# Performance work log

Measured on AMD Instinct MI355X. Metric: run time of the kernel, lower is better.

Reference implementation:

```python
import jax, jax.numpy as jnp
import numpy as np

LN_EPS = 1e-5

def layernorm(x, w, b):
    mu = jnp.mean(x, axis=-1, keepdims=True)
    var = jnp.mean(jnp.square(x - mu), axis=-1, keepdims=True)
    return (x - mu) * jax.lax.rsqrt(var + LN_EPS) * w + b

def l2_normalize(x, eps=1e-12):
    n = jnp.sqrt(jnp.sum(jnp.square(x), axis=-1, keepdims=True))
    return x / jnp.maximum(n, eps)

def setup_inputs() -> dict:
    key = jax.random.key(0)
    k1, k2 = jax.random.split(key)
    B, D, Npix = 8, 64, 32768
    K, P = 19, 5
    return {
        "base_feature": jax.random.normal(k1, (B, D, Npix), dtype=jnp.float32),
        "means": jax.random.normal(k2, (K, P, D), dtype=jnp.float32) * 0.02,  # trunc_normal_(std=0.02)
        "diagonal": jnp.ones((K, P, D), dtype=jnp.float32),
        "feat_w": jnp.ones((D,), dtype=jnp.float32),
        "feat_b": jnp.zeros((D,), dtype=jnp.float32),
        "mask_w": jnp.ones((K,), dtype=jnp.float32),
        "mask_b": jnp.zeros((K,), dtype=jnp.float32),
    }

def gmm_log_prob(x, mu, scale):
    # x: [N, D]; mu, scale: [KP, D]  (MultivariateNormalDiag with scale_diag=scale)
    # log p = -0.5 * sum(((x-mu)/s)^2) - sum(log s) - 0.5*D*log(2*pi)
    D = x.shape[-1]
    inv2 = 1.0 / jnp.square(scale)                      # [KP, D]
    quad = (jnp.square(x) @ inv2.T                       # [N, KP]
            - 2.0 * (x @ (mu * inv2).T)
            + jnp.sum(jnp.square(mu) * inv2, axis=-1))
    log_norm = jnp.sum(jnp.log(scale), axis=-1) + 0.5 * D * jnp.log(2.0 * jnp.pi)
    return -0.5 * quad - log_norm                        # [N, KP]

def reference(base_feature, means, diagonal, feat_w, feat_b, mask_w, mask_b):
    B, D, Npix = base_feature.shape
    K, P, _ = means.shape
    # 'b c n -> (b n) c'
    _c = jnp.transpose(base_feature, (0, 2, 1)).reshape(B * Npix, D)
    _c = layernorm(_c, feat_w, feat_b)
    _c = l2_normalize(_c)
    means_n = l2_normalize(means)                        # means.data.copy_(l2_normalize(means))
    logp = gmm_log_prob(_c, means_n.reshape(K * P, D), diagonal.reshape(K * P, D))
    final_probs = logp.reshape(-1, K, P)                 # [(b n), K, P]
    _m_prob = jnp.max(final_probs, axis=-1)              # amax over components -> [(b n), K]
    out_seg = layernorm(_m_prob, mask_w, mask_b)         # mask_norm
    # '(b n) k -> b k n'
    out_seg = jnp.transpose(out_seg.reshape(B, Npix, K), (0, 2, 1))
    return out_seg
```

## Files before the change

### kernel.cpp

```cpp
#include <hip/hip_runtime.h>
#include <math.h>

#define BB    8
#define DD    64
#define NPIX  32768
#define KK    19
#define PP    5
#define KP    95
#define KPAD  96

typedef _Float16 half8 __attribute__((ext_vector_type(8)));
typedef float f32x4 __attribute__((ext_vector_type(4)));

#define ROW_B   528
#define SLOT_B  8448
#define UT_B    33792
#define SCR_OFF 33792
#define LDS_B   36352

__global__ __launch_bounds__(64) void gmm_prep(
        const float* __restrict__ means, const float* __restrict__ diag,
        const float* __restrict__ feat_w, const float* __restrict__ feat_b,
        _Float16* __restrict__ Ch, _Float16* __restrict__ Cl,
        float* __restrict__ cst, float* __restrict__ scal) {
    int j = blockIdx.x;
    int d = threadIdx.x;
    if (j < KP) {
        float mu = means[j * DD + d];
        float sc = diag[j * DD + d];
        float ss = mu * mu;
        #pragma unroll
        for (int off = 32; off; off >>= 1) ss += __shfl_xor(ss, off);
        float inv = 1.f / fmaxf(sqrtf(ss), 1e-12f);
        float mn = mu * inv;
        float i2 = 1.f / (sc * sc);
        float A = mn * i2;
        float B = -0.5f * i2;
        _Float16 ah = (_Float16)A; _Float16 al = (_Float16)(A - (float)ah);
        _Float16 bh = (_Float16)B; _Float16 bl = (_Float16)(B - (float)bh);
        Ch[j * 128 + 2 * d]     = ah;
        Ch[j * 128 + 2 * d + 1] = bh;
        Cl[j * 128 + 2 * d]     = al;
        Cl[j * 128 + 2 * d + 1] = bl;
        float c1 = mn * mn * i2;
        float c2 = logf(sc);
        #pragma unroll
        for (int off = 32; off; off >>= 1) {
            c1 += __shfl_xor(c1, off);
            c2 += __shfl_xor(c2, off);
        }
        if (d == 0) cst[j] = -0.5f * c1 - c2 - 58.8120661251f;
    } else {
        Ch[95 * 128 + 2 * d] = (_Float16)0.f; Ch[95 * 128 + 2 * d + 1] = (_Float16)0.f;
        Cl[95 * 128 + 2 * d] = (_Float16)0.f; Cl[95 * 128 + 2 * d + 1] = (_Float16)0.f;
        float w = feat_w[d], b = feat_b[d];
        float s0 = w * w, s1 = w * b, s2 = b * b;
        #pragma unroll
        for (int off = 32; off; off >>= 1) {
            s0 += __shfl_xor(s0, off);
            s1 += __shfl_xor(s1, off);
            s2 += __shfl_xor(s2, off);
        }
        if (d == 0) { cst[95] = 0.f; scal[0] = s0; scal[1] = s1; scal[2] = s2; }
    }
}

__global__ __launch_bounds__(128, 2) void gmm_main(
        const float* __restrict__ bf,
        const float* __restrict__ feat_w, const float* __restrict__ feat_b,
        const float* __restrict__ mask_w, const float* __restrict__ mask_b,
        const _Float16* __restrict__ Ch, const _Float16* __restrict__ Cl,
        const float* __restrict__ cst, const float* __restrict__ scal,
        float* __restrict__ out) {
    __shared__ __align__(16) unsigned char smem[LDS_B];
    float* scratch = (float*)(smem + SCR_OFF);

    const int tid  = threadIdx.x;
    const int w    = tid >> 6;
    const int lane = tid & 63;
    const int m15  = lane & 15;
    const int q    = lane >> 4;
    const int bidx = blockIdx.x;
    const int b    = bidx >> 9;
    const int n0   = (bidx & 511) << 6;

    half8 Ahf[3][4], Alf[3][4];
    #pragma unroll
    for (int t = 0; t < 3; ++t) {
        const int row = (3 * w + t) * 16 + m15;
        #pragma unroll
        for (int ks = 0; ks < 4; ++ks) {
            Ahf[t][ks] = *(const half8*)(Ch + row * 128 + ks * 32 + q * 8);
            Alf[t][ks] = *(const half8*)(Cl + row * 128 + ks * 32 + q * 8);
        }
    }

    const int dbase = w * 32;
    const float* xp = bf + (size_t)b * (DD * NPIX) + (size_t)dbase * NPIX + n0 + lane;
    float xs[32];
    #pragma unroll
    for (int i = 0; i < 32; ++i) xs[i] = xp[(size_t)i * NPIX];

    float S1 = 0.f, S2 = 0.f, S3 = 0.f, S4 = 0.f, S5 = 0.f;
    #pragma unroll
    for (int i = 0; i < 32; ++i) {
        float wd = feat_w[dbase + i];
        float bd = feat_b[dbase + i];
        float x  = xs[i];
        float t  = wd * x;
        S1 += x;
        S2 = fmaf(x, x, S2);
        S3 = fmaf(t, t, S3);
        S4 = fmaf(t, wd, S4);
        S5 = fmaf(t, bd, S5);
    }
    scratch[w * 320 +   0 + lane] = S1;
    scratch[w * 320 +  64 + lane] = S2;
    scratch[w * 320 + 128 + lane] = S3;
    scratch[w * 320 + 192 + lane] = S4;
    scratch[w * 320 + 256 + lane] = S5;
    __syncthreads();
    {
        const int ow = (1 - w) * 320;
        S1 += scratch[ow +   0 + lane];
        S2 += scratch[ow +  64 + lane];
        S3 += scratch[ow + 128 + lane];
        S4 += scratch[ow + 192 + lane];
        S5 += scratch[ow + 256 + lane];
    }
    const float W2 = scal[0], WB = scal[1], B2 = scal[2];
    float mu  = S1 * (1.f / 64.f);
    float var = fmaxf(S2 * (1.f / 64.f) - mu * mu, 0.f);
    float r   = rsqrtf(var + 1e-5f);
    float Sy2 = r * r * (S3 - 2.f * mu * S4 + mu * mu * W2)
              + 2.f * r * (S5 - mu * WB) + B2;
    float nrm  = sqrtf(fmaxf(Sy2, 0.f));
    float invn = 1.f / fmaxf(nrm, 1e-12f);
    float alpha = invn * r;
    float e = invn;
    float f = -alpha * mu;

    {
        unsigned char* rowp = smem + lane * ROW_B;
        #pragma unroll
        for (int g = 0; g < 8; ++g) {
            half8 vh, vl;
            #pragma unroll
            for (int jj = 0; jj < 4; ++jj) {
                int d = dbase + 4 * g + jj;
                float wd = feat_w[d];
                float bd = feat_b[d];
                float c  = fmaf(f, wd, e * bd);
                float u  = fmaf(alpha * wd, xs[4 * g + jj], c);
                float us = u * u;
                _Float16 uh = (_Float16)u;  _Float16 ul = (_Float16)(u  - (float)uh);
                _Float16 qh = (_Float16)us; _Float16 ql = (_Float16)(us - (float)qh);
                vh[2 * jj] = uh; vh[2 * jj + 1] = qh;
                vl[2 * jj] = ul; vl[2 * jj + 1] = ql;
            }
            *(half8*)(rowp + 4 * (dbase + 4 * g))       = vh;
            *(half8*)(rowp + 256 + 4 * (dbase + 4 * g)) = vl;
        }
    }
    __syncthreads();

    #pragma unroll 1
    for (int s = 0; s < 4; ++s) {
        const unsigned ubase = (unsigned)(s * 16 + m15) * ROW_B + q * 16;
        half8 Uh[4], Ul[4];
        #pragma unroll
        for (int ks = 0; ks < 4; ++ks) {
            Uh[ks] = *(const half8*)(smem + ubase + ks * 64);
            Ul[ks] = *(const half8*)(smem + ubase + 256 + ks * 64);
        }
        __syncthreads();

        f32x4 a0 = {0.f, 0.f, 0.f, 0.f}, a1 = a0, a2 = a0;
        #pragma unroll
        for (int ks = 0; ks < 4; ++ks) {
            a0 = __builtin_amdgcn_mfma_f32_16x16x32_f16(Ahf[0][ks], Uh[ks], a0, 0, 0, 0);
            a1 = __builtin_amdgcn_mfma_f32_16x16x32_f16(Ahf[1][ks], Uh[ks], a1, 0, 0, 0);
            a2 = __builtin_amdgcn_mfma_f32_16x16x32_f16(Ahf[2][ks], Uh[ks], a2, 0, 0, 0);
        }
        #pragma unroll
        for (int ks = 0; ks < 4; ++ks) {
            a0 = __builtin_amdgcn_mfma_f32_16x16x32_f16(Ahf[0][ks], Ul[ks], a0, 0, 0, 0);
            a1 = __builtin_amdgcn_mfma_f32_16x16x32_f16(Ahf[1][ks], Ul[ks], a1, 0, 0, 0);
            a2 = __builtin_amdgcn_mfma_f32_16x16x32_f16(Ahf[2][ks], Ul[ks], a2, 0, 0, 0);
        }
        #pragma unroll
        for (int ks = 0; ks < 4; ++ks) {
            a0 = __builtin_amdgcn_mfma_f32_16x16x32_f16(Alf[0][ks], Uh[ks], a0, 0, 0, 0);
            a1 = __builtin_amdgcn_mfma_f32_16x16x32_f16(Alf[1][ks], Uh[ks], a1, 0, 0, 0);
            a2 = __builtin_amdgcn_mfma_f32_16x16x32_f16(Alf[2][ks], Uh[ks], a2, 0, 0, 0);
        }

        unsigned char* slotp = smem + s * SLOT_B + s * 64;
        #pragma unroll
        for (int rg = 0; rg < 4; ++rg) {
            int j0 = (3 * w + 0) * 16 + q * 4 + rg;
            int j1 = (3 * w + 1) * 16 + q * 4 + rg;
            int j2 = (3 * w + 2) * 16 + q * 4 + rg;
            *(float*)(slotp + (j0 * 17 + m15) * 4) = a0[rg];
            *(float*)(slotp + (j1 * 17 + m15) * 4) = a1[rg];
            *(float*)(slotp + (j2 * 17 + m15) * 4) = a2[rg];
        }
    }
    __syncthreads();

    if ((lane & 32) == 0) {
        int px   = w * 32 + (lane & 31);
        int slot = px >> 4;
        int col  = px & 15;
        const unsigned char* sb = smem + slot * SLOT_B + slot * 64;
        float m[KK];
        #pragma unroll
        for (int k = 0; k < KK; ++k) {
            float best = -3.4e38f;
            #pragma unroll
            for (int p = 0; p < PP; ++p) {
                int j = 5 * k + p;
                float v = *(const float*)(sb + (j * 17 + col) * 4) + cst[j];
                best = fmaxf(best, v);
            }
            m[k] = best;
        }
        float mum = 0.f;
        #pragma unroll
        for (int k = 0; k < KK; ++k) mum += m[k];
        mum *= (1.f / 19.f);
        float varm = 0.f;
        #pragma unroll
        for (int k = 0; k < KK; ++k) { float t = m[k] - mum; varm = fmaf(t, t, varm); }
        varm *= (1.f / 19.f);
        float rm = rsqrtf(varm + 1e-5f);
        float* op = out + (size_t)b * (KK * NPIX) + n0 + px;
        #pragma unroll
        for (int k = 0; k < KK; ++k)
            op[(size_t)k * NPIX] = (m[k] - mum) * rm * mask_w[k] + mask_b[k];
    }
}

extern "C" void kernel_launch(void* const* d_in, const int* in_sizes, int n_in,
                              void* d_out, int out_size, void* d_ws, size_t ws_size,
                              hipStream_t stream) {
    const float* base_feature = (const float*)d_in[0];
    const float* means        = (const float*)d_in[1];
    const float* diagonal     = (const float*)d_in[2];
    const float* feat_w       = (const float*)d_in[3];
    const float* feat_b       = (const float*)d_in[4];
    const float* mask_w       = (const float*)d_in[5];
    const float* mask_b       = (const float*)d_in[6];
    float* out = (float*)d_out;

    _Float16* Ch = (_Float16*)d_ws;
    _Float16* Cl = Ch + KPAD * 128;
    float* cst   = (float*)(Cl + KPAD * 128);
    float* scal  = cst + KPAD;

    gmm_prep<<<KPAD, 64, 0, stream>>>(means, diagonal, feat_w, feat_b, Ch, Cl, cst, scal);

    gmm_main<<<(BB * NPIX) / 64, 128, 0, stream>>>(
        base_feature, feat_w, feat_b, mask_w, mask_b, Ch, Cl, cst, scal, out);
}
```

Measured before the change: 147.1 us.

## Make each wave own 32 pixels independently, removing block barriers and LDS sharing

Each wave now processes its own 32 pixels. The two half-waves split the 64 channels and combine their partial layernorm statistics with cross-lane shuffles instead of an LDS exchange and barriers. The GMM coefficient fragments are streamed from global memory per 16-component tile, not held in registers, and the U tile uses an XOR-swizzled LDS layout to avoid bank conflicts. The final max/layernorm stage is split across both half-waves, so all lanes stay busy. In exchange, the coefficient matrix is reloaded per wave from cache, and each wave now does all 96 columns of MFMA work.

```diff
diff --git a/kernel.cpp b/kernel.cpp
--- a/kernel.cpp
+++ b/kernel.cpp
@@ -12,11 +12,7 @@
 typedef _Float16 half8 __attribute__((ext_vector_type(8)));
 typedef float f32x4 __attribute__((ext_vector_type(4)));
 
-#define ROW_B   528
-#define SLOT_B  8448
-#define UT_B    33792
-#define SCR_OFF 33792
-#define LDS_B   36352
+#define WAVE_LDS 16384
 
 __global__ __launch_bounds__(64) void gmm_prep(
         const float* __restrict__ means, const float* __restrict__ diag,
@@ -72,31 +68,22 @@
         const _Float16* __restrict__ Ch, const _Float16* __restrict__ Cl,
         const float* __restrict__ cst, const float* __restrict__ scal,
         float* __restrict__ out) {
-    __shared__ __align__(16) unsigned char smem[LDS_B];
-    float* scratch = (float*)(smem + SCR_OFF);
+    __shared__ __align__(16) unsigned char smem[2 * WAVE_LDS];
 
     const int tid  = threadIdx.x;
     const int w    = tid >> 6;
     const int lane = tid & 63;
+    const int px   = lane & 31;
+    const int h    = lane >> 5;
     const int m15  = lane & 15;
     const int q    = lane >> 4;
     const int bidx = blockIdx.x;
     const int b    = bidx >> 9;
-    const int n0   = (bidx & 511) << 6;
-
-    half8 Ahf[3][4], Alf[3][4];
-    #pragma unroll
-    for (int t = 0; t < 3; ++t) {
-        const int row = (3 * w + t) * 16 + m15;
-        #pragma unroll
-        for (int ks = 0; ks < 4; ++ks) {
-            Ahf[t][ks] = *(const half8*)(Ch + row * 128 + ks * 32 + q * 8);
-            Alf[t][ks] = *(const half8*)(Cl + row * 128 + ks * 32 + q * 8);
-        }
-    }
-
-    const int dbase = w * 32;
-    const float* xp = bf + (size_t)b * (DD * NPIX) + (size_t)dbase * NPIX + n0 + lane;
+    const int n0   = ((bidx & 511) << 6) + (w << 5);
+    unsigned char* wbase = smem + w * WAVE_LDS;
+
+    const int dbase = h * 32;
+    const float* xp = bf + (size_t)b * (DD * NPIX) + (size_t)dbase * NPIX + n0 + px;
     float xs[32];
     #pragma unroll
     for (int i = 0; i < 32; ++i) xs[i] = xp[(size_t)i * NPIX];
@@ -114,34 +101,25 @@
         S4 = fmaf(t, wd, S4);
         S5 = fmaf(t, bd, S5);
     }
-    scratch[w * 320 +   0 + lane] = S1;
-    scratch[w * 320 +  64 + lane] = S2;
-    scratch[w * 320 + 128 + lane] = S3;
-    scratch[w * 320 + 192 + lane] = S4;
-    scratch[w * 320 + 256 + lane] = S5;
-    __syncthreads();
-    {
-        const int ow = (1 - w) * 320;
-        S1 += scratch[ow +   0 + lane];
-        S2 += scratch[ow +  64 + lane];
-        S3 += scratch[ow + 128 + lane];
-        S4 += scratch[ow + 192 + lane];
-        S5 += scratch[ow + 256 + lane];
-    }
+    S1 += __shfl_xor(S1, 32);
+    S2 += __shfl_xor(S2, 32);
+    S3 += __shfl_xor(S3, 32);
+    S4 += __shfl_xor(S4, 32);
+    S5 += __shfl_xor(S5, 32);
+
     const float W2 = scal[0], WB = scal[1], B2 = scal[2];
     float mu  = S1 * (1.f / 64.f);
     float var = fmaxf(S2 * (1.f / 64.f) - mu * mu, 0.f);
     float r   = rsqrtf(var + 1e-5f);
     float Sy2 = r * r * (S3 - 2.f * mu * S4 + mu * mu * W2)
               + 2.f * r * (S5 - mu * WB) + B2;
-    float nrm  = sqrtf(fmaxf(Sy2, 0.f));
-    float invn = 1.f / fmaxf(nrm, 1e-12f);
+    float invn  = 1.f / fmaxf(sqrtf(fmaxf(Sy2, 0.f)), 1e-12f);
     float alpha = invn * r;
     float e = invn;
     float f = -alpha * mu;
 
     {
-        unsigned char* rowp = smem + lane * ROW_B;
+        unsigned char* rowp = wbase + px * 512;
         #pragma unroll
         for (int g = 0; g < 8; ++g) {
             half8 vh, vl;
@@ -158,86 +136,92 @@
                 vh[2 * jj] = uh; vh[2 * jj + 1] = qh;
                 vl[2 * jj] = ul; vl[2 * jj + 1] = ql;
             }
-            *(half8*)(rowp + 4 * (dbase + 4 * g))       = vh;
-            *(half8*)(rowp + 256 + 4 * (dbase + 4 * g)) = vl;
-        }
-    }
-    __syncthreads();
-
-    #pragma unroll 1
-    for (int s = 0; s < 4; ++s) {
-        const unsigned ubase = (unsigned)(s * 16 + m15) * ROW_B + q * 16;
-        half8 Uh[4], Ul[4];
-        #pragma unroll
-        for (int ks = 0; ks < 4; ++ks) {
-            Uh[ks] = *(const half8*)(smem + ubase + ks * 64);
-            Ul[ks] = *(const half8*)(smem + ubase + 256 + ks * 64);
-        }
-        __syncthreads();
-
-        f32x4 a0 = {0.f, 0.f, 0.f, 0.f}, a1 = a0, a2 = a0;
-        #pragma unroll
-        for (int ks = 0; ks < 4; ++ks) {
-            a0 = __builtin_amdgcn_mfma_f32_16x16x32_f16(Ahf[0][ks], Uh[ks], a0, 0, 0, 0);
-            a1 = __builtin_amdgcn_mfma_f32_16x16x32_f16(Ahf[1][ks], Uh[ks], a1, 0, 0, 0);
-            a2 = __builtin_amdgcn_mfma_f32_16x16x32_f16(Ahf[2][ks], Uh[ks], a2, 0, 0, 0);
-        }
-        #pragma unroll
-        for (int ks = 0; ks < 4; ++ks) {
-            a0 = __builtin_amdgcn_mfma_f32_16x16x32_f16(Ahf[0][ks], Ul[ks], a0, 0, 0, 0);
-            a1 = __builtin_amdgcn_mfma_f32_16x16x32_f16(Ahf[1][ks], Ul[ks], a1, 0, 0, 0);
-            a2 = __builtin_amdgcn_mfma_f32_16x16x32_f16(Ahf[2][ks], Ul[ks], a2, 0, 0, 0);
-        }
-        #pragma unroll
-        for (int ks = 0; ks < 4; ++ks) {
-            a0 = __builtin_amdgcn_mfma_f32_16x16x32_f16(Alf[0][ks], Uh[ks], a0, 0, 0, 0);
-            a1 = __builtin_amdgcn_mfma_f32_16x16x32_f16(Alf[1][ks], Uh[ks], a1, 0, 0, 0);
-            a2 = __builtin_amdgcn_mfma_f32_16x16x32_f16(Alf[2][ks], Uh[ks], a2, 0, 0, 0);
-        }
-
-        unsigned char* slotp = smem + s * SLOT_B + s * 64;
+            const int col = (8 * h + g) ^ (px & 15);
+            *(half8*)(rowp + (col << 4))       = vh;
+            *(half8*)(rowp + 256 + (col << 4)) = vl;
+        }
+    }
+
+    half8 Uh[2][4], Ul[2][4];
+    #pragma unroll
+    for (int pt = 0; pt < 2; ++pt) {
+        #pragma unroll
+        for (int ks = 0; ks < 4; ++ks) {
+            const int row  = pt * 16 + m15;
+            const int coli = (4 * ks + q) ^ m15;
+            Uh[pt][ks] = *(const half8*)(wbase + row * 512 + (coli << 4));
+            Ul[pt][ks] = *(const half8*)(wbase + row * 512 + 256 + (coli << 4));
+        }
+    }
+
+    float* lp = (float*)wbase;
+    #pragma unroll 2
+    for (int t = 0; t < 6; ++t) {
+        const _Float16* chp = Ch + (size_t)(16 * t + m15) * 128 + 8 * q;
+        const _Float16* clp = Cl + (size_t)(16 * t + m15) * 128 + 8 * q;
+        half8 Ah[4], Al[4];
+        #pragma unroll
+        for (int ks = 0; ks < 4; ++ks) {
+            Ah[ks] = *(const half8*)(chp + 32 * ks);
+            Al[ks] = *(const half8*)(clp + 32 * ks);
+        }
+        f32x4 a0 = {0.f, 0.f, 0.f, 0.f}, a1 = a0;
+        #pragma unroll
+        for (int ks = 0; ks < 4; ++ks) {
+            a0 = __builtin_amdgcn_mfma_f32_16x16x32_f16(Ah[ks], Uh[0][ks], a0, 0, 0, 0);
+            a1 = __builtin_amdgcn_mfma_f32_16x16x32_f16(Ah[ks], Uh[1][ks], a1, 0, 0, 0);
+        }
+        #pragma unroll
+        for (int ks = 0; ks < 4; ++ks) {
+            a0 = __builtin_amdgcn_mfma_f32_16x16x32_f16(Ah[ks], Ul[0][ks], a0, 0, 0, 0);
+            a1 = __builtin_amdgcn_mfma_f32_16x16x32_f16(Ah[ks], Ul[1][ks], a1, 0, 0, 0);
+        }
+        #pragma unroll
+        for (int ks = 0; ks < 4; ++ks) {
+            a0 = __builtin_amdgcn_mfma_f32_16x16x32_f16(Al[ks], Uh[0][ks], a0, 0, 0, 0);
+            a1 = __builtin_amdgcn_mfma_f32_16x16x32_f16(Al[ks], Uh[1][ks], a1, 0, 0, 0);
+        }
         #pragma unroll
         for (int rg = 0; rg < 4; ++rg) {
-            int j0 = (3 * w + 0) * 16 + q * 4 + rg;
-            int j1 = (3 * w + 1) * 16 + q * 4 + rg;
-            int j2 = (3 * w + 2) * 16 + q * 4 + rg;
-            *(float*)(slotp + (j0 * 17 + m15) * 4) = a0[rg];
-            *(float*)(slotp + (j1 * 17 + m15) * 4) = a1[rg];
-            *(float*)(slotp + (j2 * 17 + m15) * 4) = a2[rg];
-        }
-    }
-    __syncthreads();
-
-    if ((lane & 32) == 0) {
-        int px   = w * 32 + (lane & 31);
-        int slot = px >> 4;
-        int col  = px & 15;
-        const unsigned char* sb = smem + slot * SLOT_B + slot * 64;
-        float m[KK];
-        #pragma unroll
-        for (int k = 0; k < KK; ++k) {
-            float best = -3.4e38f;
+            const int j = 16 * t + 4 * q + rg;
+            lp[j * 33 + m15]      = a0[rg];
+            lp[j * 33 + 16 + m15] = a1[rg];
+        }
+    }
+
+    const int kbase = h * 10;
+    float mv[10];
+    float S = 0.f;
+    #pragma unroll
+    for (int kk = 0; kk < 10; ++kk) {
+        const int k = kbase + kk;
+        float best = -3.4e38f;
+        if (k < KK) {
             #pragma unroll
             for (int p = 0; p < PP; ++p) {
-                int j = 5 * k + p;
-                float v = *(const float*)(sb + (j * 17 + col) * 4) + cst[j];
-                best = fmaxf(best, v);
+                const int j = 5 * k + p;
+                best = fmaxf(best, lp[j * 33 + px] + cst[j]);
             }
-            m[k] = best;
-        }
-        float mum = 0.f;
-        #pragma unroll
-        for (int k = 0; k < KK; ++k) mum += m[k];
-        mum *= (1.f / 19.f);
-        float varm = 0.f;
-        #pragma unroll
-        for (int k = 0; k < KK; ++k) { float t = m[k] - mum; varm = fmaf(t, t, varm); }
-        varm *= (1.f / 19.f);
-        float rm = rsqrtf(varm + 1e-5f);
-        float* op = out + (size_t)b * (KK * NPIX) + n0 + px;
-        #pragma unroll
-        for (int k = 0; k < KK; ++k)
-            op[(size_t)k * NPIX] = (m[k] - mum) * rm * mask_w[k] + mask_b[k];
+            S += best;
+        }
+        mv[kk] = best;
+    }
+    S += __shfl_xor(S, 32);
+    const float mum = S * (1.f / 19.f);
+    float V = 0.f;
+    #pragma unroll
+    for (int kk = 0; kk < 10; ++kk) {
+        if (kbase + kk < KK) { float t = mv[kk] - mum; V = fmaf(t, t, V); }
+    }
+    V += __shfl_xor(V, 32);
+    const float rm = rsqrtf(V * (1.f / 19.f) + 1e-5f);
+
+    float* op = out + (size_t)b * (KK * NPIX) + n0 + px;
+    #pragma unroll
+    for (int kk = 0; kk < 10; ++kk) {
+        const int k = kbase + kk;
+        if (k < KK)
+            op[(size_t)k * NPIX] = (mv[kk] - mum) * rm * mask_w[k] + mask_b[k];
     }
 }
 
```

New measurement: 165.4 us. 12.5% more time.
